# Kernel optimization log

Hardware: AMD Instinct MI355X
Metric: run time of the kernel (lower is better)

## Reference

```python
import jax, jax.numpy as jnp
import numpy as np

N, E, D, H, L, G, OUT = 100000, 1600000, 128, 128, 3, 512, 10


def setup_inputs() -> dict:
    key = jax.random.key(0)
    ks = jax.random.split(key, 10)
    x = jax.random.normal(ks[0], (N, D), jnp.float32)
    edge_index = jax.random.randint(ks[1], (2, E), 0, N)
    batch = jnp.sort(jax.random.randint(ks[2], (N,), 0, G))
    w = lambda k, shp: jax.random.normal(k, shp, jnp.float32) * 0.05
    return {
        "x": x, "edge_index": edge_index, "batch": batch,
        "W0": w(ks[3], (D, H)), "b0": jnp.zeros((H,), jnp.float32),
        "W1": w(ks[4], (H, H)), "b1": jnp.zeros((H,), jnp.float32),
        "W2": w(ks[5], (H, H)), "b2": jnp.zeros((H,), jnp.float32),
        "Wjk": w(ks[6], (L * H, H)), "bjk": jnp.zeros((H,), jnp.float32),
        "Wm1": w(ks[7], (H, H)), "bm1": jnp.zeros((H,), jnp.float32),
        "Wm2": w(ks[8], (H, OUT)), "bm2": jnp.zeros((OUT,), jnp.float32),
    }


def _gcn_conv(h, src, dst, dinv, W, b):
    # GCNConv: transform, then sym-normalized aggregate (incl. self-loops), then bias.
    xw = h @ W                                   # [N, H]
    norm = dinv[src] * dinv[dst]                 # [E]
    agg = jax.ops.segment_sum(xw[src] * norm[:, None], dst, num_segments=h.shape[0])
    agg = agg + xw * (dinv * dinv)[:, None]      # self-loop contribution
    return agg + b


def reference(x, edge_index, batch, W0, b0, W1, b1, W2, b2, Wjk, bjk, Wm1, bm1, Wm2, bm2):
    src, dst = edge_index[0], edge_index[1]
    # degree with self-loops (edge weight 1)
    deg = jax.ops.segment_sum(jnp.ones(src.shape[0], x.dtype), dst, num_segments=x.shape[0]) + 1.0
    dinv = jax.lax.rsqrt(deg)
    xs = []
    h = x
    for (W, b) in ((W0, b0), (W1, b1), (W2, b2)):
        h = jax.nn.relu(_gcn_conv(h, src, dst, dinv, W, b))  # relu after every conv (jk mode); dropout=identity in eval
        xs.append(h)
    h = jnp.concatenate(xs, axis=-1) @ Wjk + bjk  # JK 'cat' + projection to hidden
    pooled = jax.ops.segment_sum(h, batch, num_segments=G)  # global_add_pool -> [G, H]
    # MLP head [H, H, OUT]: Linear -> (BN ~ identity at init/eval) -> ReLU -> (dropout=id) -> Linear
    return jax.nn.relu(pooled @ Wm1 + bm1) @ Wm2 + bm2
```

## Files before the change

### kernel.cpp

```cpp
#include <hip/hip_runtime.h>

typedef __attribute__((ext_vector_type(8))) short bf16x8;
typedef __attribute__((ext_vector_type(4))) float f32x4;

#define BSHIFT 9
#define BSZ (1<<BSHIFT)
#define EPT 8

__device__ inline unsigned short f2b(float x){
    union{float f; unsigned int u;} c; c.f = x;
    unsigned int r = c.u + 0x7fffu + ((c.u >> 16) & 1u);
    return (unsigned short)(r >> 16);
}
__device__ inline float b2f_lo(unsigned int u){
    union{unsigned int u; float f;} c; c.u = u << 16; return c.f;
}
__device__ inline float b2f_hi(unsigned int u){
    union{unsigned int u; float f;} c; c.u = u & 0xffff0000u; return c.f;
}


__global__ __launch_bounds__(256) void partition_edges(const int* __restrict__ src, const int* __restrict__ dst,
                                                       int E, int* __restrict__ bcursor,
                                                       int* __restrict__ stage, int cap){
    __shared__ int lcount[256];
    __shared__ int lbase[256];
    int t = threadIdx.x;
    lcount[t] = 0;
    __syncthreads();
    int e0 = blockIdx.x*256*EPT + t;
    int b[EPT], rank[EPT], v[EPT];
    #pragma unroll
    for(int i = 0; i < EPT; ++i){
        int e = e0 + i*256;
        bool ok = e < E;
        int d = ok ? dst[e] : 0;
        int s = ok ? src[e] : 0;
        b[i] = d >> BSHIFT;
        v[i] = (s << BSHIFT) | (d & (BSZ-1));
        rank[i] = ok ? atomicAdd(&lcount[b[i]], 1) : -1;
    }
    __syncthreads();
    {
        int c = lcount[t];
        lbase[t] = (c > 0) ? atomicAdd(&bcursor[t], c) : 0;
    }
    __syncthreads();
    #pragma unroll
    for(int i = 0; i < EPT; ++i){
        if(rank[i] >= 0){
            int pos = lbase[b[i]] + rank[i];
            if(pos < cap) stage[(size_t)b[i]*cap + pos] = v[i];
        }
    }
}


__global__ __launch_bounds__(1024) void bucket_build(const int* __restrict__ stage, const int* __restrict__ bcnt,
                                                     int cap, int nb, int n,
                                                     int* __restrict__ row_start, float* __restrict__ dinv,
                                                     int* __restrict__ csr_src){
    __shared__ int hist[BSZ];
    __shared__ int red[1024];
    int b = blockIdx.x;
    int t = threadIdx.x;

    red[t] = (t < nb && t < b) ? min(bcnt[t], cap) : 0;
    __syncthreads();
    for(int s = 512; s > 0; s >>= 1){ if(t < s) red[t] += red[t+s]; __syncthreads(); }
    int bucket_base = red[0];
    __syncthreads();

    int cnt = min(bcnt[b], cap);
    const int* sp = stage + (size_t)b*cap;

    for(int i = t; i < BSZ; i += 1024) hist[i] = 0;
    __syncthreads();
    for(int i = t; i < cnt; i += 1024) atomicAdd(&hist[sp[i] & (BSZ-1)], 1);
    __syncthreads();

    int hv = (t < BSZ) ? hist[t] : 0;
    if(t < BSZ) red[t] = hv;
    __syncthreads();
    for(int s = 1; s < BSZ; s <<= 1){
        int add = (t < BSZ && t >= s) ? red[t-s] : 0;
        __syncthreads();
        if(t < BSZ) red[t] += add;
        __syncthreads();
    }
    if(t < BSZ){
        int node = (b << BSHIFT) + t;
        if(node < n){
            int start = bucket_base + red[t] - hv;
            row_start[node] = start;
            dinv[node] = rsqrtf((float)hv + 1.0f);
            hist[t] = start;
            if(node == n-1) row_start[n] = bucket_base + red[t];
        }
    }
    __syncthreads();

    for(int i = t; i < cnt; i += 1024){
        int v = sp[i];
        int p = atomicAdd(&hist[v & (BSZ-1)], 1);
        csr_src[p] = v >> BSHIFT;
    }
}


__global__ void prep_w_all(const float* __restrict__ W0, const float* __restrict__ W1,
                           const float* __restrict__ W2, const float* __restrict__ Wjk,
                           unsigned short* __restrict__ hi,
                           float* __restrict__ pooled, int* __restrict__ bcursor){
    int m = blockIdx.x >> 6;
    int i = (blockIdx.x & 63)*256 + threadIdx.x;
    int tid = blockIdx.x*256 + threadIdx.x;
    if(tid < 512*128) pooled[tid] = 0.f;
    if(tid < 256) bcursor[tid] = 0;
    const float* W = (m==0) ? W0 : (m==1) ? W1 : (m==2) ? W2 : (Wjk + (m-3)*16384);
    int k = i >> 7, c = i & 127;
    hi[(size_t)m*16384 + c*128 + (k ^ ((c & 7) << 3))] = f2b(W[i]);
}


__global__ __launch_bounds__(512) void gemm_f32A(const float* __restrict__ in,
                                                 const unsigned short* __restrict__ Wt_hi,
                                                 const float* __restrict__ dinv,
                                                 unsigned short* __restrict__ out, int n){
    __shared__ __align__(16) unsigned short Bs[16384];
    int t = threadIdx.x;
    int lane = t & 63;
    int r0 = blockIdx.x*128 + (t >> 6)*16;
    int lr = lane & 15;
    int lk = (lane >> 4) * 8;

    {
        uint4* d = (uint4*)Bs;
        const uint4* sH = (const uint4*)Wt_hi;
        #pragma unroll
        for(int i = 0; i < 4; ++i) d[t + i*512] = sH[t + i*512];
    }
    __syncthreads();

    f32x4 acc[8];
    #pragma unroll
    for(int c = 0; c < 8; ++c) acc[c] = (f32x4){0.f, 0.f, 0.f, 0.f};

    int arow_i = r0 + lr; if(arow_i > n-1) arow_i = n-1;
    const float* arow = in + (size_t)arow_i*128;

    #pragma unroll
    for(int k0 = 0; k0 < 128; k0 += 32){
        f32x4 a0 = *(const f32x4*)(arow + k0 + lk);
        f32x4 a1 = *(const f32x4*)(arow + k0 + lk + 4);
        bf16x8 ahi;
        #pragma unroll
        for(int j = 0; j < 4; ++j){
            ahi[j]   = (short)f2b(a0[j]);
            ahi[j+4] = (short)f2b(a1[j]);
        }
        int kidx = (k0 + lk) ^ ((lr & 7) << 3);
        #pragma unroll
        for(int c = 0; c < 8; ++c){
            bf16x8 bhi = *(const bf16x8*)&Bs[(c*16 + lr)*128 + kidx];
            acc[c] = __builtin_amdgcn_mfma_f32_16x16x32_bf16(ahi, bhi, acc[c], 0, 0, 0);
        }
    }

    float dv[4];
    #pragma unroll
    for(int i = 0; i < 4; ++i){
        int cr = r0 + ((lane >> 4) << 2) + i; if(cr > n-1) cr = n-1;
        dv[i] = dinv[cr];
    }
    #pragma unroll
    for(int c = 0; c < 8; ++c){
        int ccol = c*16 + lr;
        #pragma unroll
        for(int i = 0; i < 4; ++i){
            int crow = r0 + ((lane >> 4) << 2) + i;
            if(crow < n) out[(size_t)crow*128 + ccol] = f2b(acc[c][i] * dv[i]);
        }
    }
}


__global__ __launch_bounds__(512) void gemm_b16A(const unsigned short* __restrict__ in,
                                                 const unsigned short* __restrict__ Wt_hi,
                                                 const float* __restrict__ dinv,
                                                 unsigned short* __restrict__ out, int n){
    __shared__ __align__(16) unsigned short Bs[16384];
    int t = threadIdx.x;
    int lane = t & 63;
    int r0 = blockIdx.x*128 + (t >> 6)*16;
    int lr = lane & 15;
    int lk = (lane >> 4) * 8;

    {
        uint4* d = (uint4*)Bs;
        const uint4* sH = (const uint4*)Wt_hi;
        #pragma unroll
        for(int i = 0; i < 4; ++i) d[t + i*512] = sH[t + i*512];
    }
    __syncthreads();

    f32x4 acc[8];
    #pragma unroll
    for(int c = 0; c < 8; ++c) acc[c] = (f32x4){0.f, 0.f, 0.f, 0.f};

    int arow_i = r0 + lr; if(arow_i > n-1) arow_i = n-1;
    const unsigned short* arow = in + (size_t)arow_i*128;

    #pragma unroll
    for(int k0 = 0; k0 < 128; k0 += 32){
        bf16x8 ahi = *(const bf16x8*)(arow + k0 + lk);
        int kidx = (k0 + lk) ^ ((lr & 7) << 3);
        #pragma unroll
        for(int c = 0; c < 8; ++c){
            bf16x8 bhi = *(const bf16x8*)&Bs[(c*16 + lr)*128 + kidx];
            acc[c] = __builtin_amdgcn_mfma_f32_16x16x32_bf16(ahi, bhi, acc[c], 0, 0, 0);
        }
    }

    float dv[4];
    #pragma unroll
    for(int i = 0; i < 4; ++i){
        int cr = r0 + ((lane >> 4) << 2) + i; if(cr > n-1) cr = n-1;
        dv[i] = dinv[cr];
    }
    #pragma unroll
    for(int c = 0; c < 8; ++c){
        int ccol = c*16 + lr;
        #pragma unroll
        for(int i = 0; i < 4; ++i){
            int crow = r0 + ((lane >> 4) << 2) + i;
            if(crow < n) out[(size_t)crow*128 + ccol] = f2b(acc[c][i] * dv[i]);
        }
    }
}


__global__ __launch_bounds__(512) void gemm_jk_pool(const unsigned short* __restrict__ habc,
                                                    const unsigned short* __restrict__ Whi,
                                                    const float* __restrict__ bias,
                                                    const int* __restrict__ batch,
                                                    float* __restrict__ pooled, int n){
    __shared__ __align__(16) unsigned short Bs[16384];
    int t = threadIdx.x;
    int lane = t & 63;
    int r0 = blockIdx.x*128 + (t >> 6)*16;
    int lr = lane & 15;
    int lk = (lane >> 4) * 8;

    f32x4 acc[8];
    #pragma unroll
    for(int c = 0; c < 8; ++c) acc[c] = (f32x4){0.f, 0.f, 0.f, 0.f};

    int arow_i = r0 + lr; if(arow_i > n-1) arow_i = n-1;

    for(int kb3 = 0; kb3 < 3; ++kb3){
        __syncthreads();
        {
            uint4* d = (uint4*)Bs;
            const uint4* sH = (const uint4*)(Whi + (size_t)(3 + kb3)*16384);
            #pragma unroll
            for(int i = 0; i < 4; ++i) d[t + i*512] = sH[t + i*512];
        }
        __syncthreads();

        const unsigned short* arow = habc + (size_t)kb3*n*128 + (size_t)arow_i*128;
        #pragma unroll
        for(int k0 = 0; k0 < 128; k0 += 32){
            bf16x8 ahi = *(const bf16x8*)(arow + k0 + lk);
            int kidx = (k0 + lk) ^ ((lr & 7) << 3);
            #pragma unroll
            for(int c = 0; c < 8; ++c){
                bf16x8 bhi = *(const bf16x8*)&Bs[(c*16 + lr)*128 + kidx];
                acc[c] = __builtin_amdgcn_mfma_f32_16x16x32_bf16(ahi, bhi, acc[c], 0, 0, 0);
            }
        }
    }

    int rbase = r0 + ((lane >> 4) << 2);
    int g[4];
    #pragma unroll
    for(int i = 0; i < 4; ++i){
        int crow = rbase + i;
        g[i] = (crow < n) ? batch[crow] : -1;
    }
    int gf = __shfl(g[0], 0);
    bool uni = __all(g[0]==gf && g[1]==gf && g[2]==gf && g[3]==gf && gf >= 0);

    #pragma unroll
    for(int c = 0; c < 8; ++c){
        int ccol = c*16 + lr;
        float bcol = bias[ccol];
        if(uni){
            float s = (acc[c][0]+bcol) + (acc[c][1]+bcol) + (acc[c][2]+bcol) + (acc[c][3]+bcol);
            s += __shfl_xor(s, 16);
            s += __shfl_xor(s, 32);
            if(lane < 16) atomicAdd(&pooled[gf*128 + ccol], s);
        } else {
            #pragma unroll
            for(int i = 0; i < 4; ++i){
                if(g[i] >= 0) atomicAdd(&pooled[g[i]*128 + ccol], acc[c][i] + bcol);
            }
        }
    }
}


__global__ __launch_bounds__(256) void aggregate(const unsigned int* __restrict__ y, const int* __restrict__ row_start,
                                                 const int* __restrict__ csr_src, const float* __restrict__ dinv,
                                                 const float* __restrict__ bias, unsigned int* __restrict__ hout, int n){
    int wave = threadIdx.x >> 6;
    int lane = threadIdx.x & 63;
    int node = blockIdx.x*4 + wave;
    if(node >= n) return;
    int s0 = row_start[node];
    int s1 = row_start[node+1];

    unsigned int self = y[(size_t)node*64 + lane];
    float ax[8], ay[8];
    ax[0] = b2f_lo(self); ay[0] = b2f_hi(self);
    #pragma unroll
    for(int u = 1; u < 8; ++u){ ax[u] = 0.f; ay[u] = 0.f; }

    int j = s0;
    for(; j + 8 <= s1; j += 8){
        int idx[8];
        #pragma unroll
        for(int u = 0; u < 8; ++u) idx[u] = csr_src[j+u];
        #pragma unroll
        for(int u = 0; u < 8; ++u){
            unsigned int v = y[(size_t)idx[u]*64 + lane];
            ax[u] += b2f_lo(v); ay[u] += b2f_hi(v);
        }
    }
    int rem = s1 - j;
    int idx[7];
    #pragma unroll
    for(int u = 0; u < 7; ++u) idx[u] = (u < rem) ? csr_src[j+u] : node;
    #pragma unroll
    for(int u = 0; u < 7; ++u){
        unsigned int v = y[(size_t)idx[u]*64 + lane];
        if(u < rem){ ax[u] += b2f_lo(v); ay[u] += b2f_hi(v); }
    }

    float s_x = ((ax[0]+ax[1]) + (ax[2]+ax[3])) + ((ax[4]+ax[5]) + (ax[6]+ax[7]));
    float s_y = ((ay[0]+ay[1]) + (ay[2]+ay[3])) + ((ay[4]+ay[5]) + (ay[6]+ay[7]));
    float dn = dinv[node];
    float bx = bias[lane*2], by = bias[lane*2+1];
    float rx = fmaxf(fmaf(s_x, dn, bx), 0.f);
    float ry = fmaxf(fmaf(s_y, dn, by), 0.f);
    unsigned int packed = ((unsigned int)f2b(ry) << 16) | (unsigned int)f2b(rx);
    __builtin_nontemporal_store(packed, &hout[(size_t)node*64 + lane]);
}


__global__ void head_kernel(const float* __restrict__ pooled,
                            const float* __restrict__ Wm1, const float* __restrict__ bm1,
                            const float* __restrict__ Wm2, const float* __restrict__ bm2,
                            float* __restrict__ out){
    __shared__ float p[128];
    __shared__ float tq[128];
    int g = blockIdx.x, j = threadIdx.x;
    p[j] = pooled[g*128 + j];
    __syncthreads();
    float a = bm1[j];
    for(int k = 0; k < 128; ++k) a = fmaf(p[k], Wm1[k*128 + j], a);
    tq[j] = fmaxf(a, 0.f);
    __syncthreads();
    if(j < 10){
        float o = bm2[j];
        for(int k = 0; k < 128; ++k) o = fmaf(tq[k], Wm2[k*10 + j], o);
        out[g*10 + j] = o;
    }
}


extern "C" void kernel_launch(void* const* d_in, const int* in_sizes, int n_in,
                              void* d_out, int out_size, void* d_ws, size_t ws_size,
                              hipStream_t stream){
    const float* x    = (const float*)d_in[0];
    const int*   ei   = (const int*)  d_in[1];
    const int*   batch= (const int*)  d_in[2];
    const float* W0   = (const float*)d_in[3];
    const float* b0   = (const float*)d_in[4];
    const float* W1   = (const float*)d_in[5];
    const float* b1   = (const float*)d_in[6];
    const float* W2   = (const float*)d_in[7];
    const float* b2   = (const float*)d_in[8];
    const float* Wjk  = (const float*)d_in[9];
    const float* bjk  = (const float*)d_in[10];
    const float* Wm1  = (const float*)d_in[11];
    const float* bm1  = (const float*)d_in[12];
    const float* Wm2  = (const float*)d_in[13];
    const float* bm2  = (const float*)d_in[14];

    const int N = in_sizes[0] / 128;
    const int E = in_sizes[1] / 2;
    const int* src = ei;
    const int* dst = ei + E;

    const int nbuck = (N + BSZ - 1) >> BSHIFT;
    const int cap   = E/nbuck + E/(nbuck*2) + 2048;

    char* ws = (char*)d_ws;
    size_t off = 0;
    auto take = [&](size_t bytes)->char*{
        char* p = ws + off; off = (off + bytes + 255) & ~(size_t)255; return p;
    };
    unsigned short* Y    = (unsigned short*)take((size_t)N*128*2);
    unsigned short* Habc = (unsigned short*)take((size_t)3*N*128*2);
    float* dinv    = (float*)take((size_t)N*4);
    int*   row_start=(int*)  take((size_t)(N+1)*4);
    int*   csr_src = (int*)  take((size_t)E*4 + 64);
    float* pooled  = (float*)take((size_t)512*128*4);
    unsigned short* Whi = (unsigned short*)take((size_t)6*16384*2);
    int*   bcursor = (int*)  take((size_t)256*4);
    int*   stage   = (int*)  take((size_t)nbuck*cap*4);

    prep_w_all     <<<384, 256, 0, stream>>>(W0, W1, W2, Wjk, Whi, pooled, bcursor);
    partition_edges<<<(E + 256*EPT - 1)/(256*EPT), 256, 0, stream>>>(src, dst, E, bcursor, stage, cap);
    bucket_build   <<<nbuck, 1024, 0, stream>>>(stage, bcursor, cap, nbuck, N, row_start, dinv, csr_src);

    int gb = (N + 127)/128;
    int ab = (N + 3)/4;
    unsigned short* H0 = Habc;
    unsigned short* H1 = Habc + (size_t)N*128;
    unsigned short* H2 = Habc + (size_t)2*N*128;

    gemm_f32A<<<gb, 512, 0, stream>>>(x,  Whi,           dinv, Y, N);
    aggregate<<<ab, 256, 0, stream>>>((const unsigned int*)Y, row_start, csr_src, dinv, b0, (unsigned int*)H0, N);
    gemm_b16A<<<gb, 512, 0, stream>>>(H0, Whi + 1*16384, dinv, Y, N);
    aggregate<<<ab, 256, 0, stream>>>((const unsigned int*)Y, row_start, csr_src, dinv, b1, (unsigned int*)H1, N);
    gemm_b16A<<<gb, 512, 0, stream>>>(H1, Whi + 2*16384, dinv, Y, N);
    aggregate<<<ab, 256, 0, stream>>>((const unsigned int*)Y, row_start, csr_src, dinv, b2, (unsigned int*)H2, N);
    gemm_jk_pool<<<gb, 512, 0, stream>>>(Habc, Whi, bjk, batch, pooled, N);

    head_kernel<<<512, 128, 0, stream>>>(pooled, Wm1, bm1, Wm2, bm2, (float*)d_out);
}
```

Measured before the change: 346.5 us.

## Fuse JK projection slices into per-layer GEMMs and drop stored layer outputs

Each layer's GEMM now also multiplies its input by the matching slice of the JK weight and atomically pools the result per graph. The final kernel then only handles the last layer's slice. This removes the 3xN stored layer outputs and the re-read of them in the JK GEMM, and reuses the single H buffer. In exchange, LDS use per block doubles to 64KB, accumulator registers double, and there are extra atomic pooling passes.

Result: slower. 368.3 us (+6.3%).

```diff
diff --git a/kernel.cpp b/kernel.cpp
--- a/kernel.cpp
+++ b/kernel.cpp
@@ -185,10 +185,104 @@
 }
 
 
-__global__ __launch_bounds__(512) void gemm_b16A(const unsigned short* __restrict__ in,
-                                                 const unsigned short* __restrict__ Wt_hi,
-                                                 const float* __restrict__ dinv,
-                                                 unsigned short* __restrict__ out, int n){
+__global__ __launch_bounds__(512) void gemm_b16A_jk(const unsigned short* __restrict__ in,
+                                                    const unsigned short* __restrict__ Wt,
+                                                    const unsigned short* __restrict__ Wjkt,
+                                                    const float* __restrict__ dinv,
+                                                    const int* __restrict__ batch,
+                                                    unsigned short* __restrict__ out,
+                                                    float* __restrict__ pooled, int n){
+    __shared__ __align__(16) unsigned short Bs[32768];
+    int t = threadIdx.x;
+    int lane = t & 63;
+    int r0 = blockIdx.x*128 + (t >> 6)*16;
+    int lr = lane & 15;
+    int lk = (lane >> 4) * 8;
+
+    {
+        uint4* d = (uint4*)Bs;
+        const uint4* s1 = (const uint4*)Wt;
+        const uint4* s2 = (const uint4*)Wjkt;
+        #pragma unroll
+        for(int i = 0; i < 4; ++i){
+            d[t + i*512]        = s1[t + i*512];
+            d[2048 + t + i*512] = s2[t + i*512];
+        }
+    }
+    __syncthreads();
+
+    f32x4 accW[8], accJ[8];
+    #pragma unroll
+    for(int c = 0; c < 8; ++c){
+        accW[c] = (f32x4){0.f, 0.f, 0.f, 0.f};
+        accJ[c] = (f32x4){0.f, 0.f, 0.f, 0.f};
+    }
+
+    int arow_i = r0 + lr; if(arow_i > n-1) arow_i = n-1;
+    const unsigned short* arow = in + (size_t)arow_i*128;
+
+    #pragma unroll
+    for(int k0 = 0; k0 < 128; k0 += 32){
+        bf16x8 ahi = *(const bf16x8*)(arow + k0 + lk);
+        int kidx = (k0 + lk) ^ ((lr & 7) << 3);
+        #pragma unroll
+        for(int c = 0; c < 8; ++c){
+            bf16x8 bw = *(const bf16x8*)&Bs[(c*16 + lr)*128 + kidx];
+            bf16x8 bj = *(const bf16x8*)&Bs[16384 + (c*16 + lr)*128 + kidx];
+            accW[c] = __builtin_amdgcn_mfma_f32_16x16x32_bf16(ahi, bw, accW[c], 0, 0, 0);
+            accJ[c] = __builtin_amdgcn_mfma_f32_16x16x32_bf16(ahi, bj, accJ[c], 0, 0, 0);
+        }
+    }
+
+    float dv[4];
+    #pragma unroll
+    for(int i = 0; i < 4; ++i){
+        int cr = r0 + ((lane >> 4) << 2) + i; if(cr > n-1) cr = n-1;
+        dv[i] = dinv[cr];
+    }
+    #pragma unroll
+    for(int c = 0; c < 8; ++c){
+        int ccol = c*16 + lr;
+        #pragma unroll
+        for(int i = 0; i < 4; ++i){
+            int crow = r0 + ((lane >> 4) << 2) + i;
+            if(crow < n) out[(size_t)crow*128 + ccol] = f2b(accW[c][i] * dv[i]);
+        }
+    }
+
+    int rbase = r0 + ((lane >> 4) << 2);
+    int g[4];
+    #pragma unroll
+    for(int i = 0; i < 4; ++i){
+        int crow = rbase + i;
+        g[i] = (crow < n) ? batch[crow] : -1;
+    }
+    int gf = __shfl(g[0], 0);
+    bool uni = __all(g[0]==gf && g[1]==gf && g[2]==gf && g[3]==gf && gf >= 0);
+
+    #pragma unroll
+    for(int c = 0; c < 8; ++c){
+        int ccol = c*16 + lr;
+        if(uni){
+            float s = (accJ[c][0] + accJ[c][1]) + (accJ[c][2] + accJ[c][3]);
+            s += __shfl_xor(s, 16);
+            s += __shfl_xor(s, 32);
+            if(lane < 16) atomicAdd(&pooled[gf*128 + ccol], s);
+        } else {
+            #pragma unroll
+            for(int i = 0; i < 4; ++i){
+                if(g[i] >= 0) atomicAdd(&pooled[g[i]*128 + ccol], accJ[c][i]);
+            }
+        }
+    }
+}
+
+
+__global__ __launch_bounds__(512) void gemm_jk_pool1(const unsigned short* __restrict__ in,
+                                                     const unsigned short* __restrict__ Wjkt,
+                                                     const float* __restrict__ bias,
+                                                     const int* __restrict__ batch,
+                                                     float* __restrict__ pooled, int n){
     __shared__ __align__(16) unsigned short Bs[16384];
     int t = threadIdx.x;
     int lane = t & 63;
@@ -198,7 +292,7 @@
 
     {
         uint4* d = (uint4*)Bs;
-        const uint4* sH = (const uint4*)Wt_hi;
+        const uint4* sH = (const uint4*)Wjkt;
         #pragma unroll
         for(int i = 0; i < 4; ++i) d[t + i*512] = sH[t + i*512];
     }
@@ -219,65 +313,6 @@
         for(int c = 0; c < 8; ++c){
             bf16x8 bhi = *(const bf16x8*)&Bs[(c*16 + lr)*128 + kidx];
             acc[c] = __builtin_amdgcn_mfma_f32_16x16x32_bf16(ahi, bhi, acc[c], 0, 0, 0);
-        }
-    }
-
-    float dv[4];
-    #pragma unroll
-    for(int i = 0; i < 4; ++i){
-        int cr = r0 + ((lane >> 4) << 2) + i; if(cr > n-1) cr = n-1;
-        dv[i] = dinv[cr];
-    }
-    #pragma unroll
-    for(int c = 0; c < 8; ++c){
-        int ccol = c*16 + lr;
-        #pragma unroll
-        for(int i = 0; i < 4; ++i){
-            int crow = r0 + ((lane >> 4) << 2) + i;
-            if(crow < n) out[(size_t)crow*128 + ccol] = f2b(acc[c][i] * dv[i]);
-        }
-    }
-}
-
-
-__global__ __launch_bounds__(512) void gemm_jk_pool(const unsigned short* __restrict__ habc,
-                                                    const unsigned short* __restrict__ Whi,
-                                                    const float* __restrict__ bias,
-                                                    const int* __restrict__ batch,
-                                                    float* __restrict__ pooled, int n){
-    __shared__ __align__(16) unsigned short Bs[16384];
-    int t = threadIdx.x;
-    int lane = t & 63;
-    int r0 = blockIdx.x*128 + (t >> 6)*16;
-    int lr = lane & 15;
-    int lk = (lane >> 4) * 8;
-
-    f32x4 acc[8];
-    #pragma unroll
-    for(int c = 0; c < 8; ++c) acc[c] = (f32x4){0.f, 0.f, 0.f, 0.f};
-
-    int arow_i = r0 + lr; if(arow_i > n-1) arow_i = n-1;
-
-    for(int kb3 = 0; kb3 < 3; ++kb3){
-        __syncthreads();
-        {
-            uint4* d = (uint4*)Bs;
-            const uint4* sH = (const uint4*)(Whi + (size_t)(3 + kb3)*16384);
-            #pragma unroll
-            for(int i = 0; i < 4; ++i) d[t + i*512] = sH[t + i*512];
-        }
-        __syncthreads();
-
-        const unsigned short* arow = habc + (size_t)kb3*n*128 + (size_t)arow_i*128;
-        #pragma unroll
-        for(int k0 = 0; k0 < 128; k0 += 32){
-            bf16x8 ahi = *(const bf16x8*)(arow + k0 + lk);
-            int kidx = (k0 + lk) ^ ((lr & 7) << 3);
-            #pragma unroll
-            for(int c = 0; c < 8; ++c){
-                bf16x8 bhi = *(const bf16x8*)&Bs[(c*16 + lr)*128 + kidx];
-                acc[c] = __builtin_amdgcn_mfma_f32_16x16x32_bf16(ahi, bhi, acc[c], 0, 0, 0);
-            }
         }
     }
 
@@ -412,7 +447,7 @@
         char* p = ws + off; off = (off + bytes + 255) & ~(size_t)255; return p;
     };
     unsigned short* Y    = (unsigned short*)take((size_t)N*128*2);
-    unsigned short* Habc = (unsigned short*)take((size_t)3*N*128*2);
+    unsigned short* H    = (unsigned short*)take((size_t)N*128*2);
     float* dinv    = (float*)take((size_t)N*4);
     int*   row_start=(int*)  take((size_t)(N+1)*4);
     int*   csr_src = (int*)  take((size_t)E*4 + 64);
@@ -427,17 +462,14 @@
 
     int gb = (N + 127)/128;
     int ab = (N + 3)/4;
-    unsigned short* H0 = Habc;
-    unsigned short* H1 = Habc + (size_t)N*128;
-    unsigned short* H2 = Habc + (size_t)2*N*128;
-
-    gemm_f32A<<<gb, 512, 0, stream>>>(x,  Whi,           dinv, Y, N);
-    aggregate<<<ab, 256, 0, stream>>>((const unsigned int*)Y, row_start, csr_src, dinv, b0, (unsigned int*)H0, N);
-    gemm_b16A<<<gb, 512, 0, stream>>>(H0, Whi + 1*16384, dinv, Y, N);
-    aggregate<<<ab, 256, 0, stream>>>((const unsigned int*)Y, row_start, csr_src, dinv, b1, (unsigned int*)H1, N);
-    gemm_b16A<<<gb, 512, 0, stream>>>(H1, Whi + 2*16384, dinv, Y, N);
-    aggregate<<<ab, 256, 0, stream>>>((const unsigned int*)Y, row_start, csr_src, dinv, b2, (unsigned int*)H2, N);
-    gemm_jk_pool<<<gb, 512, 0, stream>>>(Habc, Whi, bjk, batch, pooled, N);
+
+    gemm_f32A  <<<gb, 512, 0, stream>>>(x, Whi, dinv, Y, N);
+    aggregate  <<<ab, 256, 0, stream>>>((const unsigned int*)Y, row_start, csr_src, dinv, b0, (unsigned int*)H, N);
+    gemm_b16A_jk<<<gb, 512, 0, stream>>>(H, Whi + 1*16384, Whi + 3*16384, dinv, batch, Y, pooled, N);
+    aggregate  <<<ab, 256, 0, stream>>>((const unsigned int*)Y, row_start, csr_src, dinv, b1, (unsigned int*)H, N);
+    gemm_b16A_jk<<<gb, 512, 0, stream>>>(H, Whi + 2*16384, Whi + 4*16384, dinv, batch, Y, pooled, N);
+    aggregate  <<<ab, 256, 0, stream>>>((const unsigned int*)Y, row_start, csr_src, dinv, b2, (unsigned int*)H, N);
+    gemm_jk_pool1<<<gb, 512, 0, stream>>>(H, Whi + 5*16384, bjk, batch, pooled, N);
 
     head_kernel<<<512, 128, 0, stream>>>(pooled, Wm1, bm1, Wm2, bm2, (float*)d_out);
 }
```
